# Kernel tuning notes

Hardware: AMD Instinct MI355X
Metric: run time of the kernel (lower is better)

Reference implementation:

```python
import jax, jax.numpy as jnp
import numpy as np

N, S, D, K = 4, 2048, 512, 16  # batch, seq_len, d_model, d_state


def setup_inputs() -> dict:
    key = jax.random.key(0)
    ks = jax.random.split(key, 6)
    tokens = jax.random.normal(ks[0], (N, S, D), dtype=jnp.float32)
    log_A = jax.random.normal(ks[1], (D, K), dtype=jnp.float32) * 0.1
    W_B = jax.random.normal(ks[2], (K, D), dtype=jnp.float32) * (1.0 / np.sqrt(D))
    W_C = jax.random.normal(ks[3], (K, D), dtype=jnp.float32) * (1.0 / np.sqrt(D))
    W_delta = jax.random.normal(ks[4], (D, D), dtype=jnp.float32) * (1.0 / np.sqrt(D))
    b_delta = jax.random.normal(ks[5], (D,), dtype=jnp.float32) * 0.01
    return {"tokens": tokens, "log_A": log_A, "W_B": W_B, "W_C": W_C,
            "W_delta": W_delta, "b_delta": b_delta}


def _selective_scan(toks, log_A, W_B, W_C, W_delta, b_delta):
    # toks: [N,S,D]
    deltas = jax.nn.softplus(toks @ W_delta.T + b_delta)          # [N,S,D]
    Bs = toks @ W_B.T                                             # [N,S,K]
    Cs = toks @ W_C.T                                             # [N,S,K]
    A_cont = -jnp.exp(log_A)                                      # [D,K]
    A_disc = jnp.exp(deltas[..., None] * A_cont)                  # [N,S,D,K]
    B_disc = deltas[..., None] * Bs[:, :, None, :]                # [N,S,D,K]

    def step(state, inp):
        a, b, x, c = inp  # a,b: [N,D,K]; x: [N,D]; c: [N,K]
        state = a * state + b * x[..., None]                      # [N,D,K]
        y = jnp.einsum('ndk,nk->nd', state, c)                    # [N,D]
        return state, y

    xs = (jnp.moveaxis(A_disc, 1, 0), jnp.moveaxis(B_disc, 1, 0),
          jnp.moveaxis(toks, 1, 0), jnp.moveaxis(Cs, 1, 0))
    init = jnp.zeros((toks.shape[0], log_A.shape[0], log_A.shape[1]), toks.dtype)
    _, ys = jax.lax.scan(step, init, xs)                          # ys: [S,N,D]
    return jnp.moveaxis(ys, 0, 1)                                 # [N,S,D]


def reference(tokens, log_A, W_B, W_C, W_delta, b_delta):
    out_fwd = _selective_scan(tokens, log_A, W_B, W_C, W_delta, b_delta)
    out_bwd = _selective_scan(jnp.flip(tokens, axis=1), log_A, W_B, W_C, W_delta, b_delta)
    out = out_fwd + jnp.flip(out_bwd, axis=1)                     # [N,S,D]
    return out.mean(axis=1)                                       # [N,D]
```

## Files before the change

kernel.cpp:

```cpp
#include <hip/hip_runtime.h>
#include <math.h>

#define NB   4
#define SEQ  2048
#define DM   512
#define KS   16
#define ROWS (NB*SEQ)

#define NCHUNK 16
#define CLEN   (SEQ / NCHUNK)
#define CH_TOT (2 * NB * NCHUNK * DM * KS)

#define BM 64
#define BN 64
#define BK 32
#define LDP 68

__device__ __forceinline__ float softplus_f(float z) {
    return z > 20.f ? z : log1pf(__expf(z));
}

__global__ __launch_bounds__(256)
void k_delta(const float* __restrict__ toks, const float* __restrict__ Wd,
             const float* __restrict__ bd, float* __restrict__ odelta,
             float* __restrict__ odx)
{
    __shared__ float As[BK][LDP];
    __shared__ float Ws[BK][LDP];
    const int tid = threadIdx.x;
    const int rowBase = blockIdx.x * BM;
    const int colBase = blockIdx.y * BN;
    const int tr = tid >> 4;
    const int tc = tid & 15;
    const int lm = tid >> 2;
    const int le = (tid & 3) << 3;

    float acc[4][4] = {};

    const float* gA = toks + (size_t)(rowBase + lm) * DM + le;
    const float* gW = Wd   + (size_t)(colBase + lm) * DM + le;

    for (int e0 = 0; e0 < DM; e0 += BK) {
        float4 a0 = *(const float4*)(gA);
        float4 a1 = *(const float4*)(gA + 4);
        float4 w0 = *(const float4*)(gW);
        float4 w1 = *(const float4*)(gW + 4);
        gA += BK; gW += BK;

        __syncthreads();
        As[le+0][lm] = a0.x; As[le+1][lm] = a0.y; As[le+2][lm] = a0.z; As[le+3][lm] = a0.w;
        As[le+4][lm] = a1.x; As[le+5][lm] = a1.y; As[le+6][lm] = a1.z; As[le+7][lm] = a1.w;
        Ws[le+0][lm] = w0.x; Ws[le+1][lm] = w0.y; Ws[le+2][lm] = w0.z; Ws[le+3][lm] = w0.w;
        Ws[le+4][lm] = w1.x; Ws[le+5][lm] = w1.y; Ws[le+6][lm] = w1.z; Ws[le+7][lm] = w1.w;
        __syncthreads();

        #pragma unroll
        for (int e = 0; e < BK; ++e) {
            float4 av = *(const float4*)&As[e][tr << 2];
            float4 wv = *(const float4*)&Ws[e][tc << 2];
            float a_[4] = {av.x, av.y, av.z, av.w};
            float w_[4] = {wv.x, wv.y, wv.z, wv.w};
            #pragma unroll
            for (int i = 0; i < 4; ++i)
                #pragma unroll
                for (int j = 0; j < 4; ++j)
                    acc[i][j] = fmaf(a_[i], w_[j], acc[i][j]);
        }
    }

    const int d0 = colBase + (tc << 2);
    const float4 bv = *(const float4*)(bd + d0);
    #pragma unroll
    for (int i = 0; i < 4; ++i) {
        const int r = rowBase + (tr << 2) + i;
        const float4 tv = *(const float4*)(toks + (size_t)r * DM + d0);
        float4 dl, dxv;
        dl.x = softplus_f(acc[i][0] + bv.x);
        dl.y = softplus_f(acc[i][1] + bv.y);
        dl.z = softplus_f(acc[i][2] + bv.z);
        dl.w = softplus_f(acc[i][3] + bv.w);
        dxv.x = dl.x * tv.x; dxv.y = dl.y * tv.y;
        dxv.z = dl.z * tv.z; dxv.w = dl.w * tv.w;
        *(float4*)(odelta + (size_t)r * DM + d0) = dl;
        *(float4*)(odx    + (size_t)r * DM + d0) = dxv;
    }
}

__global__ __launch_bounds__(256)
void k_bc(const float* __restrict__ toks, const float* __restrict__ WB,
          const float* __restrict__ WC, float* __restrict__ oB,
          float* __restrict__ oC)
{
    const int tid = threadIdx.x;
    const int k  = tid & 15;
    const int rl = tid >> 4;
    const int row = blockIdx.x * 16 + rl;
    const float* tp = toks + (size_t)row * DM;
    const float* wb = WB + (size_t)k * DM;
    const float* wc = WC + (size_t)k * DM;
    float ab = 0.f, ac = 0.f;
    #pragma unroll 4
    for (int e = 0; e < DM; e += 4) {
        float4 tv = *(const float4*)(tp + e);
        float4 bv = *(const float4*)(wb + e);
        float4 cv = *(const float4*)(wc + e);
        ab = fmaf(tv.x, bv.x, ab); ab = fmaf(tv.y, bv.y, ab);
        ab = fmaf(tv.z, bv.z, ab); ab = fmaf(tv.w, bv.w, ab);
        ac = fmaf(tv.x, cv.x, ac); ac = fmaf(tv.y, cv.y, ac);
        ac = fmaf(tv.z, cv.z, ac); ac = fmaf(tv.w, cv.w, ac);
    }
    oB[(size_t)row * KS + k] = ab;
    oC[(size_t)row * KS + k] = ac;
}

__global__ __launch_bounds__(256)
void k_scan_chunk(const float* __restrict__ de, const float* __restrict__ dx,
                  const float* __restrict__ Bs, const float* __restrict__ Cs,
                  const float* __restrict__ logA,
                  float* __restrict__ oP, float* __restrict__ oQ,
                  float* __restrict__ oR, float* __restrict__ oS)
{
    const int g     = blockIdx.x * blockDim.x + threadIdx.x;
    const int k     = g & 15;
    const int d     = (g >> 4) & (DM - 1);
    const int chunk = (g >> 13) & (NCHUNK - 1);
    const int n     = (g >> 17) & (NB - 1);
    const int dir   = (g >> 19) & 1;

    const float Ac = -__expf(logA[d * KS + k]);

    const int sgn = dir ? -1 : 1;
    const int t0  = dir ? (SEQ - 1 - chunk * CLEN) : (chunk * CLEN);
    const size_t rbase = (size_t)n * SEQ + t0;

    const float* pd = de + rbase * DM + d;
    const float* px = dx + rbase * DM + d;
    const float* pb = Bs + rbase * KS + k;
    const float* pc = Cs + rbase * KS + k;
    const int sD = sgn * DM;
    const int sK = sgn * KS;

    float A = 1.f, u = 0.f, R = 0.f, S = 0.f;
    #pragma unroll 4
    for (int t = 0; t < CLEN; ++t) {
        const float dev = *pd;
        const float bxv = *px;
        const float bv  = *pb;
        const float cv  = *pc;
        pd += sD; px += sD; pb += sK; pc += sK;
        const float a = __expf(dev * Ac);
        u = fmaf(a, u, bxv * bv);
        A = A * a;
        R = fmaf(cv, A, R);
        S = fmaf(cv, u, S);
    }

    const size_t idx = ((((size_t)dir * NB + n) * NCHUNK + chunk) * DM + d) * KS + k;
    oP[idx] = A; oQ[idx] = u; oR[idx] = R; oS[idx] = S;
}

__global__ __launch_bounds__(256)
void k_scan_fix(const float* __restrict__ oP, const float* __restrict__ oQ,
                const float* __restrict__ oR, const float* __restrict__ oS,
                float* __restrict__ out)
{
    const int g   = blockIdx.x * blockDim.x + threadIdx.x;
    const int k   = g & 15;
    const int d   = (g >> 4) & (DM - 1);
    const int n   = (g >> 13) & (NB - 1);
    const int dir = (g >> 15) & 1;

    size_t idx = ((((size_t)dir * NB + n) * NCHUNK) * DM + d) * KS + k;
    const size_t stride = (size_t)DM * KS;

    float h = 0.f, acc = 0.f;
    #pragma unroll
    for (int c = 0; c < NCHUNK; ++c) {
        const float P = oP[idx];
        const float Q = oQ[idx];
        const float R = oR[idx];
        const float S = oS[idx];
        idx += stride;
        acc = fmaf(R, h, acc) + S;
        h   = fmaf(P, h, Q);
    }

    acc += __shfl_xor(acc, 1);
    acc += __shfl_xor(acc, 2);
    acc += __shfl_xor(acc, 4);
    acc += __shfl_xor(acc, 8);

    if (k == 0)
        atomicAdd(&out[n * DM + d], acc * (1.0f / SEQ));
}

extern "C" void kernel_launch(void* const* d_in, const int* in_sizes, int n_in,
                              void* d_out, int out_size, void* d_ws, size_t ws_size,
                              hipStream_t stream) {
    const float* toks = (const float*)d_in[0];
    const float* logA = (const float*)d_in[1];
    const float* WB   = (const float*)d_in[2];
    const float* WC   = (const float*)d_in[3];
    const float* Wd   = (const float*)d_in[4];
    const float* bd   = (const float*)d_in[5];
    float* out = (float*)d_out;

    float* ws    = (float*)d_ws;
    float* wdel  = ws;
    float* wdx   = wdel + (size_t)ROWS * DM;
    float* wB    = wdx  + (size_t)ROWS * DM;
    float* wC    = wB   + (size_t)ROWS * KS;
    float* wP    = wC   + (size_t)ROWS * KS;
    float* wQ    = wP   + (size_t)CH_TOT;
    float* wR    = wQ   + (size_t)CH_TOT;
    float* wS    = wR   + (size_t)CH_TOT;

    hipMemsetAsync(d_out, 0, sizeof(float) * NB * DM, stream);

    k_delta<<<dim3(ROWS / BM, DM / BN), 256, 0, stream>>>(toks, Wd, bd, wdel, wdx);
    k_bc<<<ROWS / 16, 256, 0, stream>>>(toks, WB, WC, wB, wC);
    k_scan_chunk<<<(2 * NB * NCHUNK * DM * KS) / 256, 256, 0, stream>>>(
        wdel, wdx, wB, wC, logA, wP, wQ, wR, wS);
    k_scan_fix<<<(2 * NB * DM * KS) / 256, 256, 0, stream>>>(wP, wQ, wR, wS, out);
}
```

Measured before the change: 278.0 us.

## Fuse B/C projections into delta GEMM with larger tiles and register prefetch

Removes the separate k_bc kernel by adding a ninth column-block to the delta GEMM grid that computes the B and C projections (32 output columns, zero-padded to 64). The GEMM tile grows to 128x64 with BK=16 and 8x4 outputs per thread, and the next K-slice of global loads is prefetched into registers while the current tile is computed. This saves one launch and a separate pass over the tokens, at the cost of wasted FMAs on the padded BC block and higher register pressure.

```diff
diff --git a/kernel.cpp b/kernel.cpp
--- a/kernel.cpp
+++ b/kernel.cpp
@@ -11,111 +11,121 @@
 #define CLEN   (SEQ / NCHUNK)
 #define CH_TOT (2 * NB * NCHUNK * DM * KS)
 
-#define BM 64
+#define BM 128
 #define BN 64
-#define BK 32
-#define LDP 68
+#define BK 16
+#define LDA (BM + 4)
+#define LDB (BN + 4)
 
 __device__ __forceinline__ float softplus_f(float z) {
     return z > 20.f ? z : log1pf(__expf(z));
 }
 
 __global__ __launch_bounds__(256)
-void k_delta(const float* __restrict__ toks, const float* __restrict__ Wd,
-             const float* __restrict__ bd, float* __restrict__ odelta,
-             float* __restrict__ odx)
+void k_delta_fused(const float* __restrict__ toks, const float* __restrict__ Wd,
+                   const float* __restrict__ WB,   const float* __restrict__ WC,
+                   const float* __restrict__ bd,
+                   float* __restrict__ odelta, float* __restrict__ odx,
+                   float* __restrict__ oB,     float* __restrict__ oC)
 {
-    __shared__ float As[BK][LDP];
-    __shared__ float Ws[BK][LDP];
+    __shared__ float As[BK][LDA];
+    __shared__ float Bs[BK][LDB];
     const int tid = threadIdx.x;
     const int rowBase = blockIdx.x * BM;
-    const int colBase = blockIdx.y * BN;
-    const int tr = tid >> 4;
-    const int tc = tid & 15;
-    const int lm = tid >> 2;
-    const int le = (tid & 3) << 3;
-
-    float acc[4][4] = {};
-
-    const float* gA = toks + (size_t)(rowBase + lm) * DM + le;
-    const float* gW = Wd   + (size_t)(colBase + lm) * DM + le;
+    const int by   = blockIdx.y;
+    const bool isBC = (by == 8);
+    const int colBase = by * BN;
+
+    const int tm = tid >> 4;
+    const int tn = tid & 15;
+
+    const int lrow = tid >> 2;
+    const int lgrp = tid & 3;
+
+    const float* gA0 = toks + (size_t)(rowBase + lrow) * DM + lgrp * 4;
+    const float* gA1 = gA0 + (size_t)64 * DM;
+
+    bool bvalid;
+    const float* gB;
+    if (!isBC) {
+        bvalid = true;
+        gB = Wd + (size_t)(colBase + lrow) * DM + lgrp * 4;
+    } else {
+        bvalid = (lrow < 32);
+        const float* base = (lrow < 16) ? (WB + (size_t)lrow * DM)
+                                        : (WC + (size_t)(lrow - 16) * DM);
+        gB = base + lgrp * 4;
+    }
+
+    float acc[8][4] = {};
+
+    float4 pa0 = *(const float4*)(gA0);
+    float4 pa1 = *(const float4*)(gA1);
+    float4 pb  = make_float4(0.f, 0.f, 0.f, 0.f);
+    if (bvalid) pb = *(const float4*)(gB);
 
     for (int e0 = 0; e0 < DM; e0 += BK) {
-        float4 a0 = *(const float4*)(gA);
-        float4 a1 = *(const float4*)(gA + 4);
-        float4 w0 = *(const float4*)(gW);
-        float4 w1 = *(const float4*)(gW + 4);
-        gA += BK; gW += BK;
-
         __syncthreads();
-        As[le+0][lm] = a0.x; As[le+1][lm] = a0.y; As[le+2][lm] = a0.z; As[le+3][lm] = a0.w;
-        As[le+4][lm] = a1.x; As[le+5][lm] = a1.y; As[le+6][lm] = a1.z; As[le+7][lm] = a1.w;
-        Ws[le+0][lm] = w0.x; Ws[le+1][lm] = w0.y; Ws[le+2][lm] = w0.z; Ws[le+3][lm] = w0.w;
-        Ws[le+4][lm] = w1.x; Ws[le+5][lm] = w1.y; Ws[le+6][lm] = w1.z; Ws[le+7][lm] = w1.w;
+        As[lgrp*4+0][lrow]    = pa0.x; As[lgrp*4+1][lrow]    = pa0.y;
+        As[lgrp*4+2][lrow]    = pa0.z; As[lgrp*4+3][lrow]    = pa0.w;
+        As[lgrp*4+0][lrow+64] = pa1.x; As[lgrp*4+1][lrow+64] = pa1.y;
+        As[lgrp*4+2][lrow+64] = pa1.z; As[lgrp*4+3][lrow+64] = pa1.w;
+        Bs[lgrp*4+0][lrow]    = pb.x;  Bs[lgrp*4+1][lrow]    = pb.y;
+        Bs[lgrp*4+2][lrow]    = pb.z;  Bs[lgrp*4+3][lrow]    = pb.w;
         __syncthreads();
+
+        if (e0 + BK < DM) {
+            pa0 = *(const float4*)(gA0 + e0 + BK);
+            pa1 = *(const float4*)(gA1 + e0 + BK);
+            if (bvalid) pb = *(const float4*)(gB + e0 + BK);
+        }
 
         #pragma unroll
         for (int e = 0; e < BK; ++e) {
-            float4 av = *(const float4*)&As[e][tr << 2];
-            float4 wv = *(const float4*)&Ws[e][tc << 2];
-            float a_[4] = {av.x, av.y, av.z, av.w};
-            float w_[4] = {wv.x, wv.y, wv.z, wv.w};
+            const float4 a0 = *(const float4*)&As[e][tm * 8];
+            const float4 a1 = *(const float4*)&As[e][tm * 8 + 4];
+            const float4 bf = *(const float4*)&Bs[e][tn * 4];
+            const float av[8] = {a0.x, a0.y, a0.z, a0.w, a1.x, a1.y, a1.z, a1.w};
+            const float bv[4] = {bf.x, bf.y, bf.z, bf.w};
             #pragma unroll
-            for (int i = 0; i < 4; ++i)
+            for (int i = 0; i < 8; ++i)
                 #pragma unroll
                 for (int j = 0; j < 4; ++j)
-                    acc[i][j] = fmaf(a_[i], w_[j], acc[i][j]);
-        }
-    }
-
-    const int d0 = colBase + (tc << 2);
-    const float4 bv = *(const float4*)(bd + d0);
-    #pragma unroll
-    for (int i = 0; i < 4; ++i) {
-        const int r = rowBase + (tr << 2) + i;
-        const float4 tv = *(const float4*)(toks + (size_t)r * DM + d0);
-        float4 dl, dxv;
-        dl.x = softplus_f(acc[i][0] + bv.x);
-        dl.y = softplus_f(acc[i][1] + bv.y);
-        dl.z = softplus_f(acc[i][2] + bv.z);
-        dl.w = softplus_f(acc[i][3] + bv.w);
-        dxv.x = dl.x * tv.x; dxv.y = dl.y * tv.y;
-        dxv.z = dl.z * tv.z; dxv.w = dl.w * tv.w;
-        *(float4*)(odelta + (size_t)r * DM + d0) = dl;
-        *(float4*)(odx    + (size_t)r * DM + d0) = dxv;
-    }
-}
-
-__global__ __launch_bounds__(256)
-void k_bc(const float* __restrict__ toks, const float* __restrict__ WB,
-          const float* __restrict__ WC, float* __restrict__ oB,
-          float* __restrict__ oC)
-{
-    const int tid = threadIdx.x;
-    const int k  = tid & 15;
-    const int rl = tid >> 4;
-    const int row = blockIdx.x * 16 + rl;
-    const float* tp = toks + (size_t)row * DM;
-    const float* wb = WB + (size_t)k * DM;
-    const float* wc = WC + (size_t)k * DM;
-    float ab = 0.f, ac = 0.f;
-    #pragma unroll 4
-    for (int e = 0; e < DM; e += 4) {
-        float4 tv = *(const float4*)(tp + e);
-        float4 bv = *(const float4*)(wb + e);
-        float4 cv = *(const float4*)(wc + e);
-        ab = fmaf(tv.x, bv.x, ab); ab = fmaf(tv.y, bv.y, ab);
-        ab = fmaf(tv.z, bv.z, ab); ab = fmaf(tv.w, bv.w, ab);
-        ac = fmaf(tv.x, cv.x, ac); ac = fmaf(tv.y, cv.y, ac);
-        ac = fmaf(tv.z, cv.z, ac); ac = fmaf(tv.w, cv.w, ac);
-    }
-    oB[(size_t)row * KS + k] = ab;
-    oC[(size_t)row * KS + k] = ac;
+                    acc[i][j] = fmaf(av[i], bv[j], acc[i][j]);
+        }
+    }
+
+    if (!isBC) {
+        const int c0 = colBase + tn * 4;
+        const float4 bv = *(const float4*)(bd + c0);
+        #pragma unroll
+        for (int i = 0; i < 8; ++i) {
+            const int r = rowBase + tm * 8 + i;
+            const float4 tv = *(const float4*)(toks + (size_t)r * DM + c0);
+            float4 dl, dxv;
+            dl.x = softplus_f(acc[i][0] + bv.x);
+            dl.y = softplus_f(acc[i][1] + bv.y);
+            dl.z = softplus_f(acc[i][2] + bv.z);
+            dl.w = softplus_f(acc[i][3] + bv.w);
+            dxv.x = dl.x * tv.x; dxv.y = dl.y * tv.y;
+            dxv.z = dl.z * tv.z; dxv.w = dl.w * tv.w;
+            *(float4*)(odelta + (size_t)r * DM + c0) = dl;
+            *(float4*)(odx    + (size_t)r * DM + c0) = dxv;
+        }
+    } else if (tn < 8) {
+        float* dst = (tn < 4) ? (oB + tn * 4) : (oC + (tn - 4) * 4);
+        #pragma unroll
+        for (int i = 0; i < 8; ++i) {
+            const int r = rowBase + tm * 8 + i;
+            *(float4*)(dst + (size_t)r * KS) =
+                make_float4(acc[i][0], acc[i][1], acc[i][2], acc[i][3]);
+        }
+    }
 }
 
 __global__ __launch_bounds__(256)
 void k_scan_chunk(const float* __restrict__ de, const float* __restrict__ dx,
-                  const float* __restrict__ Bs, const float* __restrict__ Cs,
+                  const float* __restrict__ Bsp, const float* __restrict__ Csp,
                   const float* __restrict__ logA,
                   float* __restrict__ oP, float* __restrict__ oQ,
                   float* __restrict__ oR, float* __restrict__ oS)
@@ -133,10 +143,10 @@
     const int t0  = dir ? (SEQ - 1 - chunk * CLEN) : (chunk * CLEN);
     const size_t rbase = (size_t)n * SEQ + t0;
 
-    const float* pd = de + rbase * DM + d;
-    const float* px = dx + rbase * DM + d;
-    const float* pb = Bs + rbase * KS + k;
-    const float* pc = Cs + rbase * KS + k;
+    const float* pd = de  + rbase * DM + d;
+    const float* px = dx  + rbase * DM + d;
+    const float* pb = Bsp + rbase * KS + k;
+    const float* pc = Csp + rbase * KS + k;
     const int sD = sgn * DM;
     const int sK = sgn * KS;
 
@@ -217,8 +227,8 @@
 
     hipMemsetAsync(d_out, 0, sizeof(float) * NB * DM, stream);
 
-    k_delta<<<dim3(ROWS / BM, DM / BN), 256, 0, stream>>>(toks, Wd, bd, wdel, wdx);
-    k_bc<<<ROWS / 16, 256, 0, stream>>>(toks, WB, WC, wB, wC);
+    k_delta_fused<<<dim3(ROWS / BM, 9), 256, 0, stream>>>(
+        toks, Wd, WB, WC, bd, wdel, wdx, wB, wC);
     k_scan_chunk<<<(2 * NB * NCHUNK * DM * KS) / 256, 256, 0, stream>>>(
         wdel, wdx, wB, wC, logA, wP, wQ, wR, wS);
     k_scan_fix<<<(2 * NB * DM * KS) / 256, 256, 0, stream>>>(wP, wQ, wR, wS, out);
```

Result: faster. 233.2 us (-16.1%).

## Compute delta projection with bf16 MFMA GEMM and pre-cast weights

Applied to the files above, without the earlier changes.

Replaces the fp32 SIMT tiled GEMM for the delta projection with a 128x128 tile kernel that uses bf16 MFMA 16x16x32 instructions. A small pre-kernel casts W_delta to bf16, activations are converted to bf16 on the fly, and the next K-tile is prefetched into registers. This aims to cut the GEMM's compute time, at the cost of reduced precision in delta. The epilogue now stores scalars instead of float4 vectors.

```diff
diff --git a/kernel.cpp b/kernel.cpp
--- a/kernel.cpp
+++ b/kernel.cpp
@@ -11,78 +11,130 @@
 #define CLEN   (SEQ / NCHUNK)
 #define CH_TOT (2 * NB * NCHUNK * DM * KS)
 
-#define BM 64
-#define BN 64
-#define BK 32
-#define LDP 68
+typedef __attribute__((ext_vector_type(8))) short          bf16x8;
+typedef __attribute__((ext_vector_type(8))) unsigned short u16x8;
+typedef __attribute__((ext_vector_type(4))) float          f32x4;
 
 __device__ __forceinline__ float softplus_f(float z) {
     return z > 20.f ? z : log1pf(__expf(z));
 }
 
-__global__ __launch_bounds__(256)
-void k_delta(const float* __restrict__ toks, const float* __restrict__ Wd,
-             const float* __restrict__ bd, float* __restrict__ odelta,
-             float* __restrict__ odx)
-{
-    __shared__ float As[BK][LDP];
-    __shared__ float Ws[BK][LDP];
+__device__ __forceinline__ unsigned short f2bf(float f) {
+    unsigned int u = __builtin_bit_cast(unsigned int, f);
+    u += 0x7fffu + ((u >> 16) & 1u);
+    return (unsigned short)(u >> 16);
+}
+
+__global__ __launch_bounds__(256)
+void k_cast_w(const float* __restrict__ src, unsigned short* __restrict__ dst, int n)
+{
+    const int i = (blockIdx.x * 256 + threadIdx.x) * 8;
+    if (i >= n) return;
+    const float4 a = *(const float4*)(src + i);
+    const float4 b = *(const float4*)(src + i + 4);
+    u16x8 v;
+    v[0] = f2bf(a.x); v[1] = f2bf(a.y); v[2] = f2bf(a.z); v[3] = f2bf(a.w);
+    v[4] = f2bf(b.x); v[5] = f2bf(b.y); v[6] = f2bf(b.z); v[7] = f2bf(b.w);
+    *(u16x8*)(dst + i) = v;
+}
+
+#define GBM 128
+#define GBN 128
+#define GBK 32
+#define PADK 40
+
+__global__ __launch_bounds__(256)
+void k_gemm_delta(const float* __restrict__ toks, const unsigned short* __restrict__ Wbf,
+                  const float* __restrict__ bd,
+                  float* __restrict__ odelta, float* __restrict__ odx)
+{
+    __shared__ unsigned short As[GBM][PADK];
+    __shared__ unsigned short Bs[GBN][PADK];
     const int tid = threadIdx.x;
-    const int rowBase = blockIdx.x * BM;
-    const int colBase = blockIdx.y * BN;
-    const int tr = tid >> 4;
-    const int tc = tid & 15;
-    const int lm = tid >> 2;
-    const int le = (tid & 3) << 3;
-
-    float acc[4][4] = {};
-
-    const float* gA = toks + (size_t)(rowBase + lm) * DM + le;
-    const float* gW = Wd   + (size_t)(colBase + lm) * DM + le;
-
-    for (int e0 = 0; e0 < DM; e0 += BK) {
-        float4 a0 = *(const float4*)(gA);
-        float4 a1 = *(const float4*)(gA + 4);
-        float4 w0 = *(const float4*)(gW);
-        float4 w1 = *(const float4*)(gW + 4);
-        gA += BK; gW += BK;
-
+    const int rowBase = blockIdx.x * GBM;
+    const int colBase = blockIdx.y * GBN;
+
+    const int l   = tid & 63;
+    const int wid = tid >> 6;
+    const int wm  = wid >> 1;
+    const int wn  = wid & 1;
+    const int lr  = l & 15;
+    const int lk  = (l >> 4) * 8;
+    const int lq  = (l >> 4) * 4;
+
+    const int srow  = tid >> 1;
+    const int skoff = (tid & 1) * 16;
+
+    const float*          gA = toks + (size_t)(rowBase + srow) * DM + skoff;
+    const unsigned short* gW = Wbf  + (size_t)(colBase + srow) * DM + skoff;
+
+    const f32x4 zero4 = {0.f, 0.f, 0.f, 0.f};
+    f32x4 acc[4][4];
+    #pragma unroll
+    for (int i = 0; i < 4; ++i)
+        #pragma unroll
+        for (int j = 0; j < 4; ++j) acc[i][j] = zero4;
+
+    float4 pa0 = *(const float4*)(gA);
+    float4 pa1 = *(const float4*)(gA + 4);
+    float4 pa2 = *(const float4*)(gA + 8);
+    float4 pa3 = *(const float4*)(gA + 12);
+    u16x8  pw0 = *(const u16x8*)(gW);
+    u16x8  pw1 = *(const u16x8*)(gW + 8);
+
+    for (int e0 = 0; e0 < DM; e0 += GBK) {
         __syncthreads();
-        As[le+0][lm] = a0.x; As[le+1][lm] = a0.y; As[le+2][lm] = a0.z; As[le+3][lm] = a0.w;
-        As[le+4][lm] = a1.x; As[le+5][lm] = a1.y; As[le+6][lm] = a1.z; As[le+7][lm] = a1.w;
-        Ws[le+0][lm] = w0.x; Ws[le+1][lm] = w0.y; Ws[le+2][lm] = w0.z; Ws[le+3][lm] = w0.w;
-        Ws[le+4][lm] = w1.x; Ws[le+5][lm] = w1.y; Ws[le+6][lm] = w1.z; Ws[le+7][lm] = w1.w;
+        u16x8 va, vb;
+        va[0] = f2bf(pa0.x); va[1] = f2bf(pa0.y); va[2] = f2bf(pa0.z); va[3] = f2bf(pa0.w);
+        va[4] = f2bf(pa1.x); va[5] = f2bf(pa1.y); va[6] = f2bf(pa1.z); va[7] = f2bf(pa1.w);
+        vb[0] = f2bf(pa2.x); vb[1] = f2bf(pa2.y); vb[2] = f2bf(pa2.z); vb[3] = f2bf(pa2.w);
+        vb[4] = f2bf(pa3.x); vb[5] = f2bf(pa3.y); vb[6] = f2bf(pa3.z); vb[7] = f2bf(pa3.w);
+        *(u16x8*)&As[srow][skoff]     = va;
+        *(u16x8*)&As[srow][skoff + 8] = vb;
+        *(u16x8*)&Bs[srow][skoff]     = pw0;
+        *(u16x8*)&Bs[srow][skoff + 8] = pw1;
         __syncthreads();
 
-        #pragma unroll
-        for (int e = 0; e < BK; ++e) {
-            float4 av = *(const float4*)&As[e][tr << 2];
-            float4 wv = *(const float4*)&Ws[e][tc << 2];
-            float a_[4] = {av.x, av.y, av.z, av.w};
-            float w_[4] = {wv.x, wv.y, wv.z, wv.w};
+        if (e0 + GBK < DM) {
+            pa0 = *(const float4*)(gA + e0 + GBK);
+            pa1 = *(const float4*)(gA + e0 + GBK + 4);
+            pa2 = *(const float4*)(gA + e0 + GBK + 8);
+            pa3 = *(const float4*)(gA + e0 + GBK + 12);
+            pw0 = *(const u16x8*)(gW + e0 + GBK);
+            pw1 = *(const u16x8*)(gW + e0 + GBK + 8);
+        }
+
+        bf16x8 af[4], bfr[4];
+        #pragma unroll
+        for (int f = 0; f < 4; ++f)
+            af[f] = *(const bf16x8*)&As[wm * 64 + f * 16 + lr][lk];
+        #pragma unroll
+        for (int f = 0; f < 4; ++f)
+            bfr[f] = *(const bf16x8*)&Bs[wn * 64 + f * 16 + lr][lk];
+
+        #pragma unroll
+        for (int fm = 0; fm < 4; ++fm)
             #pragma unroll
-            for (int i = 0; i < 4; ++i)
-                #pragma unroll
-                for (int j = 0; j < 4; ++j)
-                    acc[i][j] = fmaf(a_[i], w_[j], acc[i][j]);
+            for (int fn = 0; fn < 4; ++fn)
+                acc[fm][fn] = __builtin_amdgcn_mfma_f32_16x16x32_bf16(
+                    af[fm], bfr[fn], acc[fm][fn], 0, 0, 0);
+    }
+
+    #pragma unroll
+    for (int fn = 0; fn < 4; ++fn) {
+        const int col = colBase + wn * 64 + fn * 16 + lr;
+        const float bias = bd[col];
+        #pragma unroll
+        for (int fm = 0; fm < 4; ++fm) {
+            const int row0 = rowBase + wm * 64 + fm * 16 + lq;
+            #pragma unroll
+            for (int r = 0; r < 4; ++r) {
+                const size_t off = (size_t)(row0 + r) * DM + col;
+                const float dl = softplus_f(acc[fm][fn][r] + bias);
+                odelta[off] = dl;
+                odx[off]    = dl * toks[off];
+            }
         }
-    }
-
-    const int d0 = colBase + (tc << 2);
-    const float4 bv = *(const float4*)(bd + d0);
-    #pragma unroll
-    for (int i = 0; i < 4; ++i) {
-        const int r = rowBase + (tr << 2) + i;
-        const float4 tv = *(const float4*)(toks + (size_t)r * DM + d0);
-        float4 dl, dxv;
-        dl.x = softplus_f(acc[i][0] + bv.x);
-        dl.y = softplus_f(acc[i][1] + bv.y);
-        dl.z = softplus_f(acc[i][2] + bv.z);
-        dl.w = softplus_f(acc[i][3] + bv.w);
-        dxv.x = dl.x * tv.x; dxv.y = dl.y * tv.y;
-        dxv.z = dl.z * tv.z; dxv.w = dl.w * tv.w;
-        *(float4*)(odelta + (size_t)r * DM + d0) = dl;
-        *(float4*)(odx    + (size_t)r * DM + d0) = dxv;
     }
 }
 
@@ -115,7 +167,7 @@
 
 __global__ __launch_bounds__(256)
 void k_scan_chunk(const float* __restrict__ de, const float* __restrict__ dx,
-                  const float* __restrict__ Bs, const float* __restrict__ Cs,
+                  const float* __restrict__ Bsp, const float* __restrict__ Csp,
                   const float* __restrict__ logA,
                   float* __restrict__ oP, float* __restrict__ oQ,
                   float* __restrict__ oR, float* __restrict__ oS)
@@ -133,10 +185,10 @@
     const int t0  = dir ? (SEQ - 1 - chunk * CLEN) : (chunk * CLEN);
     const size_t rbase = (size_t)n * SEQ + t0;
 
-    const float* pd = de + rbase * DM + d;
-    const float* px = dx + rbase * DM + d;
-    const float* pb = Bs + rbase * KS + k;
-    const float* pc = Cs + rbase * KS + k;
+    const float* pd = de  + rbase * DM + d;
+    const float* px = dx  + rbase * DM + d;
+    const float* pb = Bsp + rbase * KS + k;
+    const float* pc = Csp + rbase * KS + k;
     const int sD = sgn * DM;
     const int sK = sgn * KS;
 
@@ -214,10 +266,13 @@
     float* wQ    = wP   + (size_t)CH_TOT;
     float* wR    = wQ   + (size_t)CH_TOT;
     float* wS    = wR   + (size_t)CH_TOT;
+    unsigned short* wWbf = (unsigned short*)(wS + (size_t)CH_TOT);
 
     hipMemsetAsync(d_out, 0, sizeof(float) * NB * DM, stream);
 
-    k_delta<<<dim3(ROWS / BM, DM / BN), 256, 0, stream>>>(toks, Wd, bd, wdel, wdx);
+    k_cast_w<<<(DM * DM) / (256 * 8), 256, 0, stream>>>(Wd, wWbf, DM * DM);
+    k_gemm_delta<<<dim3(ROWS / GBM, DM / GBN), 256, 0, stream>>>(
+        toks, wWbf, bd, wdel, wdx);
     k_bc<<<ROWS / 16, 256, 0, stream>>>(toks, WB, WC, wB, wC);
     k_scan_chunk<<<(2 * NB * NCHUNK * DM * KS) / 256, 256, 0, stream>>>(
         wdel, wdx, wB, wC, logA, wP, wQ, wR, wS);
```

Measured after the change: 248.9 us. 10.5% less time.
